# Kernel tuning notes

Hardware: AMD Instinct MI355X
Metric: run time of the kernel (lower is better)

## Reference

```python
import jax, jax.numpy as jnp
import numpy as np

K = 1024
D = 512
BETA = 0.25
ALPHA = 10.0
EPS_NORM = 1e-12  # torch F.normalize eps


def _l2_normalize(x):
    n = jnp.linalg.norm(x, axis=1, keepdims=True)
    return x / jnp.maximum(n, EPS_NORM)


def setup_inputs() -> dict:
    key = jax.random.key(0)
    k1, k2 = jax.random.split(key)
    latents = jax.random.normal(k1, (16384, D), dtype=jnp.float32)
    # nn.Embedding weight init: uniform(-1/K, 1/K)
    emb_weight = jax.random.uniform(k2, (K, D), dtype=jnp.float32,
                                    minval=-1.0 / K, maxval=1.0 / K)
    return {"latents": latents, "emb_weight": emb_weight}


def reference(latents, emb_weight):
    # latents: [B, D], emb_weight: [K, D]
    ln = _l2_normalize(latents)                               # [B, D]
    # torch uses embedding.weight.data -> detached for the attention path
    cb = _l2_normalize(jax.lax.stop_gradient(emb_weight))     # [K, D]
    attention = ln @ cb.T                                     # [B, K]
    soft_assign = jax.nn.softmax(ALPHA * attention, axis=1)   # [B, K]
    quantized = soft_assign @ emb_weight                      # [B, D]

    commitment_loss = jnp.mean((jax.lax.stop_gradient(quantized) - ln) ** 2)
    embedding_loss = jnp.mean((quantized - jax.lax.stop_gradient(ln)) ** 2)
    vq_loss = commitment_loss * BETA + embedding_loss

    avg_probs = jnp.mean(soft_assign, axis=0)                 # [K]
    entropy_vq = -jnp.sum(avg_probs * jnp.log(avg_probs + 1e-10))

    argm = jnp.argmax(attention, axis=1, keepdims=True)       # [B, 1] int
    one_hot = jax.nn.one_hot(argm[:, 0], K, dtype=latents.dtype)  # [B, K]
    hard_quantized = one_hot @ emb_weight                     # [B, D]
    # attention[one_hot.bool()].mean() == mean of row-max (argmax entries)
    cluster_metric = jnp.mean(jnp.max(attention, axis=1))

    return (quantized, vq_loss, entropy_vq, argm, hard_quantized,
            soft_assign, cluster_metric)
```

## Files before the change

### kernel.cpp

```cpp
#include <hip/hip_runtime.h>
#include <math.h>

#define D     512
#define KCB   1024
#define NT    256
#define NT2   512
#define ALPHA 10.0f
#define TAU   0.008f
#define PSTR  1040

typedef __attribute__((ext_vector_type(8))) short short8v;
typedef __attribute__((ext_vector_type(4))) float f32x4;
typedef unsigned short us;

__device__ __forceinline__ float wave_reduce_sum(float v) {
    #pragma unroll
    for (int off = 32; off >= 1; off >>= 1) v += __shfl_xor(v, off, 64);
    return v;
}

__device__ __forceinline__ short bf16r(float x) {
    union { float f; unsigned u; } c; c.f = x;
    unsigned r = (c.u + 0x7FFFu + ((c.u >> 16) & 1u)) >> 16;
    return (short)r;
}

__global__ void k_init(float* __restrict__ avg, float* __restrict__ sse, float* __restrict__ clu) {
    int t = threadIdx.x + blockIdx.x * blockDim.x;
    if (t < KCB) avg[t] = 0.0f;
    if (t == 0) { *sse = 0.0f; *clu = 0.0f; }
}

__global__ __launch_bounds__(NT) void k_prep(const float* __restrict__ emb,
                                             us* __restrict__ cb, float* __restrict__ cbinv) {
    const int k = blockIdx.x, t = threadIdx.x;
    const int wv = t >> 6, lane = t & 63;
    float2 v = ((const float2*)(emb + (size_t)k * D))[t];
    float ss = wave_reduce_sum(v.x * v.x + v.y * v.y);
    __shared__ float part[4];
    __shared__ float s_i;
    if (lane == 0) part[wv] = ss;
    __syncthreads();
    if (t == 0) s_i = 1.0f / fmaxf(sqrtf(part[0] + part[1] + part[2] + part[3]), 1e-12f);
    __syncthreads();
    float inv = s_i;
    unsigned lo = (unsigned short)bf16r(v.x * inv);
    unsigned hi = (unsigned short)bf16r(v.y * inv);
    const int d = 2 * t;
    size_t idx = (((size_t)(k >> 4) * 16 + (d >> 5)) * 64 + ((d >> 3) & 3) * 16 + (k & 15)) * 8 + (d & 7);
    ((unsigned*)cb)[idx >> 1] = lo | (hi << 16);
    if (t == 0) cbinv[k] = inv;
}

__global__ __launch_bounds__(NT) void k_tr(const float* __restrict__ emb, us* __restrict__ embT) {
    __shared__ us tile[64][65];
    const int t = threadIdx.x;
    const int k0 = (blockIdx.x & 15) * 64;
    const int d0 = (blockIdx.x >> 4) * 64;
    {
        const int r = t >> 2, cq = t & 3;
        const float4* ep = (const float4*)(emb + (size_t)(k0 + r) * D + d0 + cq * 16);
        float4 v0 = ep[0], v1 = ep[1], v2 = ep[2], v3 = ep[3];
        us* tp = &tile[r][cq * 16];
        tp[0] = (us)bf16r(v0.x); tp[1] = (us)bf16r(v0.y); tp[2] = (us)bf16r(v0.z); tp[3] = (us)bf16r(v0.w);
        tp[4] = (us)bf16r(v1.x); tp[5] = (us)bf16r(v1.y); tp[6] = (us)bf16r(v1.z); tp[7] = (us)bf16r(v1.w);
        tp[8] = (us)bf16r(v2.x); tp[9] = (us)bf16r(v2.y); tp[10] = (us)bf16r(v2.z); tp[11] = (us)bf16r(v2.w);
        tp[12] = (us)bf16r(v3.x); tp[13] = (us)bf16r(v3.y); tp[14] = (us)bf16r(v3.z); tp[15] = (us)bf16r(v3.w);
    }
    __syncthreads();
    {
        const int rd = t >> 2, kq = t & 3;
        const int dcol = d0 + rd;
        short8v w0, w1;
        #pragma unroll
        for (int j = 0; j < 8; ++j) w0[j] = (short)tile[kq * 16 + j][rd];
        #pragma unroll
        for (int j = 0; j < 8; ++j) w1[j] = (short)tile[kq * 16 + 8 + j][rd];
        const int kb0 = k0 + kq * 16, kb1 = kb0 + 8;
        size_t i0 = (((size_t)(dcol >> 4) * 32 + (kb0 >> 5)) * 64 + ((kb0 >> 3) & 3) * 16 + (dcol & 15)) * 8;
        size_t i1 = (((size_t)(dcol >> 4) * 32 + (kb1 >> 5)) * 64 + ((kb1 >> 3) & 3) * 16 + (dcol & 15)) * 8;
        *(short8v*)(embT + i0) = w0;
        *(short8v*)(embT + i1) = w1;
    }
}

__global__ __launch_bounds__(NT2, 2) void k_fused(
    const float* __restrict__ lat, const float* __restrict__ emb,
    const us* __restrict__ cb, const us* __restrict__ embT, const float* __restrict__ cbinv,
    float* __restrict__ avg_ws, float* __restrict__ clu_ws, float* __restrict__ sse_ws,
    float* __restrict__ q_out, float* __restrict__ soft_out,
    float* __restrict__ argm_out, float* __restrict__ hq_out)
{
    extern __shared__ __align__(16) us pool[];
    __shared__ float s_inv[32];
    __shared__ float s_maxp[8][32];
    __shared__ float s_amax[32];
    __shared__ float s_sump[8][32];
    __shared__ float s_den[32];
    __shared__ float s_bestv[32];
    __shared__ int   s_besti[32];
    __shared__ int   s_cnt;
    __shared__ int   s_ck[512];
    __shared__ float s_cv[512];
    __shared__ float part[8];

    const int t = threadIdx.x, wv = t >> 6, lane = t & 63;
    const int q15 = lane & 15, g = lane >> 4;
    const int b0 = blockIdx.x * 32;

    float4 ra[4], rb[4];
    #pragma unroll
    for (int i = 0; i < 4; ++i) {
        const float4* lp = (const float4*)(lat + (size_t)(b0 + wv * 4 + i) * D);
        ra[i] = lp[2 * lane]; rb[i] = lp[2 * lane + 1];
    }
    #pragma unroll
    for (int i = 0; i < 4; ++i) {
        int r = wv * 4 + i;
        float4 a = ra[i], b = rb[i];
        float ss = a.x*a.x + a.y*a.y + a.z*a.z + a.w*a.w
                 + b.x*b.x + b.y*b.y + b.z*b.z + b.w*b.w;
        ss = wave_reduce_sum(ss);
        float inv = 1.0f / fmaxf(sqrtf(ss), 1e-12f);
        short8v w;
        w[0] = bf16r(a.x * inv); w[1] = bf16r(a.y * inv);
        w[2] = bf16r(a.z * inv); w[3] = bf16r(a.w * inv);
        w[4] = bf16r(b.x * inv); w[5] = bf16r(b.y * inv);
        w[6] = bf16r(b.z * inv); w[7] = bf16r(b.w * inv);
        *(short8v*)&pool[(size_t)r * PSTR + lane * 8] = w;
        if (lane == 0) s_inv[r] = inv;
    }
    if (t == 0) s_cnt = 0;
    __syncthreads();

    f32x4 acc[2][8];
    #pragma unroll
    for (int m = 0; m < 2; ++m)
        #pragma unroll
        for (int ct = 0; ct < 8; ++ct) { f32x4 z = {0.f, 0.f, 0.f, 0.f}; acc[m][ct] = z; }

    const us* pBw = cb + (size_t)(wv * 8) * 16 * 512 + (size_t)lane * 8;
    #define LDB_A(ks, ct) (*(const short8v*)(pBw + (size_t)((ct) * 16 + (ks)) * 512))
    #define LDA_A(row, ks) (*(const short8v*)&pool[(size_t)(row) * PSTR + (ks) * 32 + g * 8])

    short8v bE[8], bO[8];
    #pragma unroll
    for (int ct = 0; ct < 8; ++ct) bE[ct] = LDB_A(0, ct);
    for (int ks = 0; ks < 16; ks += 2) {
        #pragma unroll
        for (int ct = 0; ct < 8; ++ct) bO[ct] = LDB_A(ks + 1, ct);
        short8v af0 = LDA_A(q15, ks), af1 = LDA_A(16 + q15, ks);
        #pragma unroll
        for (int ct = 0; ct < 8; ++ct) {
            acc[0][ct] = __builtin_amdgcn_mfma_f32_16x16x32_bf16(af0, bE[ct], acc[0][ct], 0, 0, 0);
            acc[1][ct] = __builtin_amdgcn_mfma_f32_16x16x32_bf16(af1, bE[ct], acc[1][ct], 0, 0, 0);
        }
        const int ksn = (ks + 2 < 16) ? ks + 2 : 0;
        #pragma unroll
        for (int ct = 0; ct < 8; ++ct) bE[ct] = LDB_A(ksn, ct);
        af0 = LDA_A(q15, ks + 1); af1 = LDA_A(16 + q15, ks + 1);
        #pragma unroll
        for (int ct = 0; ct < 8; ++ct) {
            acc[0][ct] = __builtin_amdgcn_mfma_f32_16x16x32_bf16(af0, bO[ct], acc[0][ct], 0, 0, 0);
            acc[1][ct] = __builtin_amdgcn_mfma_f32_16x16x32_bf16(af1, bO[ct], acc[1][ct], 0, 0, 0);
        }
    }

    #pragma unroll
    for (int m = 0; m < 2; ++m)
        #pragma unroll
        for (int i = 0; i < 4; ++i) {
            float v = acc[m][0][i];
            #pragma unroll
            for (int ct = 1; ct < 8; ++ct) v = fmaxf(v, acc[m][ct][i]);
            #pragma unroll
            for (int off = 8; off >= 1; off >>= 1) v = fmaxf(v, __shfl_xor(v, off, 64));
            if (q15 == 0) s_maxp[wv][m * 16 + g * 4 + i] = v;
        }
    __syncthreads();
    if (t < 32) {
        float v = s_maxp[0][t];
        #pragma unroll
        for (int w = 1; w < 8; ++w) v = fmaxf(v, s_maxp[w][t]);
        s_amax[t] = v;
    }
    __syncthreads();

    #pragma unroll
    for (int m = 0; m < 2; ++m)
        #pragma unroll
        for (int i = 0; i < 4; ++i) {
            const int row = m * 16 + g * 4 + i;
            const float thr = s_amax[row] - TAU;
            #pragma unroll
            for (int ct = 0; ct < 8; ++ct) {
                if (acc[m][ct][i] >= thr) {
                    int idx = atomicAdd(&s_cnt, 1);
                    if (idx < 512) s_ck[idx] = (row << 16) | (wv * 128 + ct * 16 + q15);
                }
            }
        }
    __syncthreads();
    const int cnt = (s_cnt < 512) ? s_cnt : 512;

    for (int e = wv; e < cnt; e += 8) {
        const int pk = s_ck[e];
        const int row = pk >> 16, kk = pk & 0xFFFF;
        const float4* lp = (const float4*)(lat + (size_t)(b0 + row) * D);
        const float4* ep = (const float4*)(emb + (size_t)kk * D);
        float4 x0 = lp[2 * lane], x1 = lp[2 * lane + 1];
        float4 y0 = ep[2 * lane], y1 = ep[2 * lane + 1];
        float dp = x0.x*y0.x + x0.y*y0.y + x0.z*y0.z + x0.w*y0.w
                 + x1.x*y1.x + x1.y*y1.y + x1.z*y1.z + x1.w*y1.w;
        dp = wave_reduce_sum(dp);
        if (lane == 0) s_cv[e] = dp * s_inv[row] * cbinv[kk];
    }
    __syncthreads();
    if (t < 32) {
        float bv = -1e30f; int bi = 0x7FFFFFFF;
        for (int e = 0; e < cnt; ++e) {
            if ((s_ck[e] >> 16) == t) {
                float v = s_cv[e]; int kk = s_ck[e] & 0xFFFF;
                if (v > bv || (v == bv && kk < bi)) { bv = v; bi = kk; }
            }
        }
        s_bestv[t] = bv; s_besti[t] = bi;
        argm_out[b0 + t] = (float)bi;
    }
    __syncthreads();

    #pragma unroll
    for (int m = 0; m < 2; ++m)
        #pragma unroll
        for (int i = 0; i < 4; ++i) {
            const float bvv = s_bestv[m * 16 + g * 4 + i];
            float s = 0.f;
            #pragma unroll
            for (int ct = 0; ct < 8; ++ct) {
                float e = __expf(ALPHA * (acc[m][ct][i] - bvv));
                acc[m][ct][i] = e;
                s += e;
            }
            #pragma unroll
            for (int off = 8; off >= 1; off >>= 1) s += __shfl_xor(s, off, 64);
            if (q15 == 0) s_sump[wv][m * 16 + g * 4 + i] = s;
        }
    __syncthreads();
    if (t < 32) {
        float s = s_sump[0][t];
        #pragma unroll
        for (int w = 1; w < 8; ++w) s += s_sump[w][t];
        s_den[t] = 1.0f / s;
    }
    __syncthreads();

    float csum[8];
    #pragma unroll
    for (int ct = 0; ct < 8; ++ct) csum[ct] = 0.f;
    #pragma unroll
    for (int m = 0; m < 2; ++m)
        #pragma unroll
        for (int i = 0; i < 4; ++i) {
            const int row = m * 16 + g * 4 + i;
            const float dn = s_den[row];
            float* orow = soft_out + (size_t)(b0 + row) * KCB + wv * 128 + q15;
            us* prow = &pool[(size_t)row * PSTR + wv * 128 + q15];
            #pragma unroll
            for (int ct = 0; ct < 8; ++ct) {
                float sv = acc[m][ct][i] * dn;
                orow[ct * 16] = sv;
                prow[ct * 16] = (us)bf16r(sv);
                csum[ct] += sv;
            }
        }
    #pragma unroll
    for (int ct = 0; ct < 8; ++ct) {
        float v = csum[ct];
        v += __shfl_xor(v, 16, 64);
        v += __shfl_xor(v, 32, 64);
        csum[ct] = v;
    }
    if (lane < 16) {
        #pragma unroll
        for (int ct = 0; ct < 8; ++ct)
            atomicAdd(avg_ws + wv * 128 + ct * 16 + lane, csum[ct]);
    }
    if (t == 0) {
        float cs = 0.f;
        #pragma unroll
        for (int r = 0; r < 32; ++r) cs += s_bestv[r];
        atomicAdd(clu_ws, cs);
    }
    __syncthreads();

    const float4* emb4 = (const float4*)emb;
    #pragma unroll
    for (int u = 0; u < 8; ++u) {
        int idx = t + u * NT2;
        int r = idx >> 7, c = idx & 127;
        ((float4*)(hq_out + (size_t)(b0 + r) * D))[c] = emb4[(size_t)s_besti[r] * 128 + c];
    }

    f32x4 qac[2][4];
    #pragma unroll
    for (int m = 0; m < 2; ++m)
        #pragma unroll
        for (int ct = 0; ct < 4; ++ct) { f32x4 z = {0.f, 0.f, 0.f, 0.f}; qac[m][ct] = z; }

    const us* pBq = embT + (size_t)(wv * 128) * 512 + (size_t)lane * 8;
    #define LDB_Q(ks, ct) (*(const short8v*)(pBq + (size_t)((ct) * 32 + (ks)) * 512))
    #define LDA_Q(row, ks) (*(const short8v*)&pool[(size_t)(row) * PSTR + (ks) * 32 + g * 8])

    short8v qE[4], qO[4];
    #pragma unroll
    for (int ct = 0; ct < 4; ++ct) qE[ct] = LDB_Q(0, ct);
    for (int ks = 0; ks < 32; ks += 2) {
        #pragma unroll
        for (int ct = 0; ct < 4; ++ct) qO[ct] = LDB_Q(ks + 1, ct);
        short8v af0 = LDA_Q(q15, ks), af1 = LDA_Q(16 + q15, ks);
        #pragma unroll
        for (int ct = 0; ct < 4; ++ct) {
            qac[0][ct] = __builtin_amdgcn_mfma_f32_16x16x32_bf16(af0, qE[ct], qac[0][ct], 0, 0, 0);
            qac[1][ct] = __builtin_amdgcn_mfma_f32_16x16x32_bf16(af1, qE[ct], qac[1][ct], 0, 0, 0);
        }
        const int ksn = (ks + 2 < 32) ? ks + 2 : 0;
        #pragma unroll
        for (int ct = 0; ct < 4; ++ct) qE[ct] = LDB_Q(ksn, ct);
        af0 = LDA_Q(q15, ks + 1); af1 = LDA_Q(16 + q15, ks + 1);
        #pragma unroll
        for (int ct = 0; ct < 4; ++ct) {
            qac[0][ct] = __builtin_amdgcn_mfma_f32_16x16x32_bf16(af0, qO[ct], qac[0][ct], 0, 0, 0);
            qac[1][ct] = __builtin_amdgcn_mfma_f32_16x16x32_bf16(af1, qO[ct], qac[1][ct], 0, 0, 0);
        }
    }

    float sse = 0.f;
    #pragma unroll
    for (int m = 0; m < 2; ++m)
        #pragma unroll
        for (int i = 0; i < 4; ++i) {
            const int rloc = m * 16 + g * 4 + i;
            const int row = b0 + rloc;
            const float rv = s_inv[rloc];
            const float* lrow = lat + (size_t)row * D + wv * 64 + q15;
            float* qrow = q_out + (size_t)row * D + wv * 64 + q15;
            #pragma unroll
            for (int ct = 0; ct < 4; ++ct) {
                float qv = qac[m][ct][i];
                qrow[ct * 16] = qv;
                float df = qv - lrow[ct * 16] * rv;
                sse += df * df;
            }
        }
    sse = wave_reduce_sum(sse);
    if (lane == 0) part[wv] = sse;
    __syncthreads();
    if (t == 0) {
        float s = 0.f;
        #pragma unroll
        for (int w = 0; w < 8; ++w) s += part[w];
        atomicAdd(sse_ws, s);
    }
    #undef LDB_A
    #undef LDA_A
    #undef LDB_Q
    #undef LDA_Q
}

__global__ __launch_bounds__(NT) void k_final(
    const float* __restrict__ avg_ws, const float* __restrict__ sse_ws, const float* __restrict__ clu_ws,
    float* __restrict__ out_vq, float* __restrict__ out_ent, float* __restrict__ out_cm,
    float invB, float invBD)
{
    const int t = threadIdx.x;
    float ent = 0.f;
    for (int idx = t; idx < KCB; idx += NT) {
        float pv = avg_ws[idx] * invB;
        ent -= pv * logf(pv + 1e-10f);
    }
    ent = wave_reduce_sum(ent);
    __shared__ float part[4];
    const int wv = t >> 6, lane = t & 63;
    if (lane == 0) part[wv] = ent;
    __syncthreads();
    if (t == 0) {
        *out_ent = part[0] + part[1] + part[2] + part[3];
        *out_vq  = 1.25f * (*sse_ws) * invBD;
        *out_cm  = (*clu_ws) * invB;
    }
}

extern "C" void kernel_launch(void* const* d_in, const int* in_sizes, int n_in,
                              void* d_out, int out_size, void* d_ws, size_t ws_size,
                              hipStream_t stream)
{
    const float* lat = (const float*)d_in[0];
    const float* emb = (const float*)d_in[1];
    const int B = in_sizes[0] / D;
    float* out = (float*)d_out;

    const size_t vq_off   = (size_t)B * D;
    const size_t ent_off  = vq_off + 1;
    const size_t argm_off = vq_off + 2;
    const size_t hq_off   = argm_off + (size_t)B;
    const size_t soft_off = hq_off + (size_t)B * D;
    const size_t cm_off   = soft_off + (size_t)B * KCB;

    us* cb_bf   = (us*)d_ws;
    us* embT_bf = cb_bf + (size_t)KCB * D;
    float* fbase  = (float*)(embT_bf + (size_t)D * KCB);
    float* cbinv  = fbase;
    float* avg_ws = cbinv + KCB;
    float* sse_ws = avg_ws + KCB;
    float* clu_ws = sse_ws + 1;

    const int lds_bytes = 32 * PSTR * 2;

    k_init<<<4, NT, 0, stream>>>(avg_ws, sse_ws, clu_ws);
    k_prep<<<KCB, NT, 0, stream>>>(emb, cb_bf, cbinv);
    k_tr<<<(D / 64) * (KCB / 64), NT, 0, stream>>>(emb, embT_bf);
    k_fused<<<B / 32, NT2, lds_bytes, stream>>>(lat, emb, cb_bf, embT_bf, cbinv,
                                                avg_ws, clu_ws, sse_ws,
                                                out, out + soft_off, out + argm_off, out + hq_off);
    k_final<<<1, NT, 0, stream>>>(avg_ws, sse_ws, clu_ws,
                                  out + vq_off, out + ent_off, out + cm_off,
                                  1.0f / (float)B, 1.0f / ((float)B * (float)D));
}
```

Before: 294.3 us.

## Double row tile to 64, merge prep kernels, and replace avg atomics with partials

The fused kernel now handles 64 latent rows per block instead of 32. Each codebook B-fragment loaded from global memory is reused across four M-tiles, which halves codebook traffic per row. The init, normalize and transpose prep kernels are merged into one launch that writes the transposed bf16 codebook with scattered 2-byte stores. Per-column soft-assignment sums go to a per-block partial buffer reduced by a new k_avg kernel when workspace allows, instead of global atomics. The cost is more accumulator registers, twice the LDS per block at a 2-block occupancy target, and half as many blocks.

```diff
diff --git a/kernel.cpp b/kernel.cpp
--- a/kernel.cpp
+++ b/kernel.cpp
@@ -5,6 +5,7 @@
 #define KCB   1024
 #define NT    256
 #define NT2   512
+#define RB    64
 #define ALPHA 10.0f
 #define TAU   0.008f
 #define PSTR  1040
@@ -25,16 +26,16 @@
     return (short)r;
 }
 
-__global__ void k_init(float* __restrict__ avg, float* __restrict__ sse, float* __restrict__ clu) {
-    int t = threadIdx.x + blockIdx.x * blockDim.x;
-    if (t < KCB) avg[t] = 0.0f;
-    if (t == 0) { *sse = 0.0f; *clu = 0.0f; }
-}
-
-__global__ __launch_bounds__(NT) void k_prep(const float* __restrict__ emb,
-                                             us* __restrict__ cb, float* __restrict__ cbinv) {
+__global__ __launch_bounds__(NT) void k_prep2(const float* __restrict__ emb,
+                                              us* __restrict__ cb, us* __restrict__ embT,
+                                              float* __restrict__ cbinv,
+                                              float* __restrict__ avg_ws,
+                                              float* __restrict__ sse, float* __restrict__ clu) {
     const int k = blockIdx.x, t = threadIdx.x;
     const int wv = t >> 6, lane = t & 63;
+    if (k < 4) avg_ws[k * NT + t] = 0.0f;
+    if (k == 0 && t == 0) { *sse = 0.0f; *clu = 0.0f; }
+
     float2 v = ((const float2*)(emb + (size_t)k * D))[t];
     float ss = wave_reduce_sum(v.x * v.x + v.y * v.y);
     __shared__ float part[4];
@@ -44,79 +45,51 @@
     if (t == 0) s_i = 1.0f / fmaxf(sqrtf(part[0] + part[1] + part[2] + part[3]), 1e-12f);
     __syncthreads();
     float inv = s_i;
+    const int d = 2 * t;
     unsigned lo = (unsigned short)bf16r(v.x * inv);
     unsigned hi = (unsigned short)bf16r(v.y * inv);
-    const int d = 2 * t;
     size_t idx = (((size_t)(k >> 4) * 16 + (d >> 5)) * 64 + ((d >> 3) & 3) * 16 + (k & 15)) * 8 + (d & 7);
     ((unsigned*)cb)[idx >> 1] = lo | (hi << 16);
+    size_t j0 = (((size_t)(d >> 4) * 32 + (k >> 5)) * 64 + ((k >> 3) & 3) * 16 + (d & 15)) * 8 + (k & 7);
+    embT[j0]     = (us)bf16r(v.x);
+    embT[j0 + 8] = (us)bf16r(v.y);
     if (t == 0) cbinv[k] = inv;
-}
-
-__global__ __launch_bounds__(NT) void k_tr(const float* __restrict__ emb, us* __restrict__ embT) {
-    __shared__ us tile[64][65];
-    const int t = threadIdx.x;
-    const int k0 = (blockIdx.x & 15) * 64;
-    const int d0 = (blockIdx.x >> 4) * 64;
-    {
-        const int r = t >> 2, cq = t & 3;
-        const float4* ep = (const float4*)(emb + (size_t)(k0 + r) * D + d0 + cq * 16);
-        float4 v0 = ep[0], v1 = ep[1], v2 = ep[2], v3 = ep[3];
-        us* tp = &tile[r][cq * 16];
-        tp[0] = (us)bf16r(v0.x); tp[1] = (us)bf16r(v0.y); tp[2] = (us)bf16r(v0.z); tp[3] = (us)bf16r(v0.w);
-        tp[4] = (us)bf16r(v1.x); tp[5] = (us)bf16r(v1.y); tp[6] = (us)bf16r(v1.z); tp[7] = (us)bf16r(v1.w);
-        tp[8] = (us)bf16r(v2.x); tp[9] = (us)bf16r(v2.y); tp[10] = (us)bf16r(v2.z); tp[11] = (us)bf16r(v2.w);
-        tp[12] = (us)bf16r(v3.x); tp[13] = (us)bf16r(v3.y); tp[14] = (us)bf16r(v3.z); tp[15] = (us)bf16r(v3.w);
-    }
-    __syncthreads();
-    {
-        const int rd = t >> 2, kq = t & 3;
-        const int dcol = d0 + rd;
-        short8v w0, w1;
-        #pragma unroll
-        for (int j = 0; j < 8; ++j) w0[j] = (short)tile[kq * 16 + j][rd];
-        #pragma unroll
-        for (int j = 0; j < 8; ++j) w1[j] = (short)tile[kq * 16 + 8 + j][rd];
-        const int kb0 = k0 + kq * 16, kb1 = kb0 + 8;
-        size_t i0 = (((size_t)(dcol >> 4) * 32 + (kb0 >> 5)) * 64 + ((kb0 >> 3) & 3) * 16 + (dcol & 15)) * 8;
-        size_t i1 = (((size_t)(dcol >> 4) * 32 + (kb1 >> 5)) * 64 + ((kb1 >> 3) & 3) * 16 + (dcol & 15)) * 8;
-        *(short8v*)(embT + i0) = w0;
-        *(short8v*)(embT + i1) = w1;
-    }
 }
 
 __global__ __launch_bounds__(NT2, 2) void k_fused(
     const float* __restrict__ lat, const float* __restrict__ emb,
     const us* __restrict__ cb, const us* __restrict__ embT, const float* __restrict__ cbinv,
-    float* __restrict__ avg_ws, float* __restrict__ clu_ws, float* __restrict__ sse_ws,
+    float* __restrict__ avg_ws, float* __restrict__ part_ws, int use_part,
+    float* __restrict__ clu_ws, float* __restrict__ sse_ws,
     float* __restrict__ q_out, float* __restrict__ soft_out,
     float* __restrict__ argm_out, float* __restrict__ hq_out)
 {
     extern __shared__ __align__(16) us pool[];
-    __shared__ float s_inv[32];
-    __shared__ float s_maxp[8][32];
-    __shared__ float s_amax[32];
-    __shared__ float s_sump[8][32];
-    __shared__ float s_den[32];
-    __shared__ float s_bestv[32];
-    __shared__ int   s_besti[32];
+    __shared__ float s_inv[RB];
+    __shared__ float s_maxp[8][RB];
+    __shared__ float s_amax[RB];
+    __shared__ float s_sump[8][RB];
+    __shared__ float s_den[RB];
+    __shared__ float s_bestv[RB];
+    __shared__ int   s_besti[RB];
     __shared__ int   s_cnt;
-    __shared__ int   s_ck[512];
-    __shared__ float s_cv[512];
+    __shared__ int   s_ck[1024];
+    __shared__ float s_cv[1024];
     __shared__ float part[8];
 
     const int t = threadIdx.x, wv = t >> 6, lane = t & 63;
     const int q15 = lane & 15, g = lane >> 4;
-    const int b0 = blockIdx.x * 32;
-
-    float4 ra[4], rb[4];
-    #pragma unroll
-    for (int i = 0; i < 4; ++i) {
-        const float4* lp = (const float4*)(lat + (size_t)(b0 + wv * 4 + i) * D);
+    const int b0 = blockIdx.x * RB;
+
+    float4 ra[8], rb[8];
+    #pragma unroll
+    for (int i = 0; i < 8; ++i) {
+        const float4* lp = (const float4*)(lat + (size_t)(b0 + wv * 8 + i) * D);
         ra[i] = lp[2 * lane]; rb[i] = lp[2 * lane + 1];
     }
     #pragma unroll
-    for (int i = 0; i < 4; ++i) {
-        int r = wv * 4 + i;
+    for (int i = 0; i < 8; ++i) {
+        int r = wv * 8 + i;
         float4 a = ra[i], b = rb[i];
         float ss = a.x*a.x + a.y*a.y + a.z*a.z + a.w*a.w
                  + b.x*b.x + b.y*b.y + b.z*b.z + b.w*b.w;
@@ -133,9 +106,9 @@
     if (t == 0) s_cnt = 0;
     __syncthreads();
 
-    f32x4 acc[2][8];
-    #pragma unroll
-    for (int m = 0; m < 2; ++m)
+    f32x4 acc[4][8];
+    #pragma unroll
+    for (int m = 0; m < 4; ++m)
         #pragma unroll
         for (int ct = 0; ct < 8; ++ct) { f32x4 z = {0.f, 0.f, 0.f, 0.f}; acc[m][ct] = z; }
 
@@ -149,25 +122,35 @@
     for (int ks = 0; ks < 16; ks += 2) {
         #pragma unroll
         for (int ct = 0; ct < 8; ++ct) bO[ct] = LDB_A(ks + 1, ct);
-        short8v af0 = LDA_A(q15, ks), af1 = LDA_A(16 + q15, ks);
-        #pragma unroll
-        for (int ct = 0; ct < 8; ++ct) {
-            acc[0][ct] = __builtin_amdgcn_mfma_f32_16x16x32_bf16(af0, bE[ct], acc[0][ct], 0, 0, 0);
-            acc[1][ct] = __builtin_amdgcn_mfma_f32_16x16x32_bf16(af1, bE[ct], acc[1][ct], 0, 0, 0);
+        {
+            short8v af0 = LDA_A(q15, ks), af1 = LDA_A(16 + q15, ks);
+            short8v af2 = LDA_A(32 + q15, ks), af3 = LDA_A(48 + q15, ks);
+            #pragma unroll
+            for (int ct = 0; ct < 8; ++ct) {
+                acc[0][ct] = __builtin_amdgcn_mfma_f32_16x16x32_bf16(af0, bE[ct], acc[0][ct], 0, 0, 0);
+                acc[1][ct] = __builtin_amdgcn_mfma_f32_16x16x32_bf16(af1, bE[ct], acc[1][ct], 0, 0, 0);
+                acc[2][ct] = __builtin_amdgcn_mfma_f32_16x16x32_bf16(af2, bE[ct], acc[2][ct], 0, 0, 0);
+                acc[3][ct] = __builtin_amdgcn_mfma_f32_16x16x32_bf16(af3, bE[ct], acc[3][ct], 0, 0, 0);
+            }
         }
         const int ksn = (ks + 2 < 16) ? ks + 2 : 0;
         #pragma unroll
         for (int ct = 0; ct < 8; ++ct) bE[ct] = LDB_A(ksn, ct);
-        af0 = LDA_A(q15, ks + 1); af1 = LDA_A(16 + q15, ks + 1);
-        #pragma unroll
-        for (int ct = 0; ct < 8; ++ct) {
-            acc[0][ct] = __builtin_amdgcn_mfma_f32_16x16x32_bf16(af0, bO[ct], acc[0][ct], 0, 0, 0);
-            acc[1][ct] = __builtin_amdgcn_mfma_f32_16x16x32_bf16(af1, bO[ct], acc[1][ct], 0, 0, 0);
-        }
-    }
-
-    #pragma unroll
-    for (int m = 0; m < 2; ++m)
+        {
+            short8v af0 = LDA_A(q15, ks + 1), af1 = LDA_A(16 + q15, ks + 1);
+            short8v af2 = LDA_A(32 + q15, ks + 1), af3 = LDA_A(48 + q15, ks + 1);
+            #pragma unroll
+            for (int ct = 0; ct < 8; ++ct) {
+                acc[0][ct] = __builtin_amdgcn_mfma_f32_16x16x32_bf16(af0, bO[ct], acc[0][ct], 0, 0, 0);
+                acc[1][ct] = __builtin_amdgcn_mfma_f32_16x16x32_bf16(af1, bO[ct], acc[1][ct], 0, 0, 0);
+                acc[2][ct] = __builtin_amdgcn_mfma_f32_16x16x32_bf16(af2, bO[ct], acc[2][ct], 0, 0, 0);
+                acc[3][ct] = __builtin_amdgcn_mfma_f32_16x16x32_bf16(af3, bO[ct], acc[3][ct], 0, 0, 0);
+            }
+        }
+    }
+
+    #pragma unroll
+    for (int m = 0; m < 4; ++m)
         #pragma unroll
         for (int i = 0; i < 4; ++i) {
             float v = acc[m][0][i];
@@ -178,7 +161,7 @@
             if (q15 == 0) s_maxp[wv][m * 16 + g * 4 + i] = v;
         }
     __syncthreads();
-    if (t < 32) {
+    if (t < RB) {
         float v = s_maxp[0][t];
         #pragma unroll
         for (int w = 1; w < 8; ++w) v = fmaxf(v, s_maxp[w][t]);
@@ -187,7 +170,7 @@
     __syncthreads();
 
     #pragma unroll
-    for (int m = 0; m < 2; ++m)
+    for (int m = 0; m < 4; ++m)
         #pragma unroll
         for (int i = 0; i < 4; ++i) {
             const int row = m * 16 + g * 4 + i;
@@ -196,12 +179,12 @@
             for (int ct = 0; ct < 8; ++ct) {
                 if (acc[m][ct][i] >= thr) {
                     int idx = atomicAdd(&s_cnt, 1);
-                    if (idx < 512) s_ck[idx] = (row << 16) | (wv * 128 + ct * 16 + q15);
+                    if (idx < 1024) s_ck[idx] = (row << 16) | (wv * 128 + ct * 16 + q15);
                 }
             }
         }
     __syncthreads();
-    const int cnt = (s_cnt < 512) ? s_cnt : 512;
+    const int cnt = (s_cnt < 1024) ? s_cnt : 1024;
 
     for (int e = wv; e < cnt; e += 8) {
         const int pk = s_ck[e];
@@ -216,7 +199,7 @@
         if (lane == 0) s_cv[e] = dp * s_inv[row] * cbinv[kk];
     }
     __syncthreads();
-    if (t < 32) {
+    if (t < RB) {
         float bv = -1e30f; int bi = 0x7FFFFFFF;
         for (int e = 0; e < cnt; ++e) {
             if ((s_ck[e] >> 16) == t) {
@@ -230,7 +213,7 @@
     __syncthreads();
 
     #pragma unroll
-    for (int m = 0; m < 2; ++m)
+    for (int m = 0; m < 4; ++m)
         #pragma unroll
         for (int i = 0; i < 4; ++i) {
             const float bvv = s_bestv[m * 16 + g * 4 + i];
@@ -246,7 +229,7 @@
             if (q15 == 0) s_sump[wv][m * 16 + g * 4 + i] = s;
         }
     __syncthreads();
-    if (t < 32) {
+    if (t < RB) {
         float s = s_sump[0][t];
         #pragma unroll
         for (int w = 1; w < 8; ++w) s += s_sump[w][t];
@@ -258,7 +241,7 @@
     #pragma unroll
     for (int ct = 0; ct < 8; ++ct) csum[ct] = 0.f;
     #pragma unroll
-    for (int m = 0; m < 2; ++m)
+    for (int m = 0; m < 4; ++m)
         #pragma unroll
         for (int i = 0; i < 4; ++i) {
             const int row = m * 16 + g * 4 + i;
@@ -280,30 +263,38 @@
         v += __shfl_xor(v, 32, 64);
         csum[ct] = v;
     }
-    if (lane < 16) {
-        #pragma unroll
-        for (int ct = 0; ct < 8; ++ct)
-            atomicAdd(avg_ws + wv * 128 + ct * 16 + lane, csum[ct]);
+    if (use_part) {
+        if (lane < 16) {
+            #pragma unroll
+            for (int ct = 0; ct < 8; ++ct)
+                part_ws[(size_t)blockIdx.x * KCB + wv * 128 + ct * 16 + lane] = csum[ct];
+        }
+    } else {
+        if (lane < 16) {
+            #pragma unroll
+            for (int ct = 0; ct < 8; ++ct)
+                atomicAdd(avg_ws + wv * 128 + ct * 16 + lane, csum[ct]);
+        }
     }
     if (t == 0) {
         float cs = 0.f;
         #pragma unroll
-        for (int r = 0; r < 32; ++r) cs += s_bestv[r];
+        for (int r = 0; r < RB; ++r) cs += s_bestv[r];
         atomicAdd(clu_ws, cs);
     }
     __syncthreads();
 
     const float4* emb4 = (const float4*)emb;
     #pragma unroll
-    for (int u = 0; u < 8; ++u) {
+    for (int u = 0; u < 16; ++u) {
         int idx = t + u * NT2;
         int r = idx >> 7, c = idx & 127;
         ((float4*)(hq_out + (size_t)(b0 + r) * D))[c] = emb4[(size_t)s_besti[r] * 128 + c];
     }
 
-    f32x4 qac[2][4];
-    #pragma unroll
-    for (int m = 0; m < 2; ++m)
+    f32x4 qac[4][4];
+    #pragma unroll
+    for (int m = 0; m < 4; ++m)
         #pragma unroll
         for (int ct = 0; ct < 4; ++ct) { f32x4 z = {0.f, 0.f, 0.f, 0.f}; qac[m][ct] = z; }
 
@@ -317,26 +308,36 @@
     for (int ks = 0; ks < 32; ks += 2) {
         #pragma unroll
         for (int ct = 0; ct < 4; ++ct) qO[ct] = LDB_Q(ks + 1, ct);
-        short8v af0 = LDA_Q(q15, ks), af1 = LDA_Q(16 + q15, ks);
-        #pragma unroll
-        for (int ct = 0; ct < 4; ++ct) {
-            qac[0][ct] = __builtin_amdgcn_mfma_f32_16x16x32_bf16(af0, qE[ct], qac[0][ct], 0, 0, 0);
-            qac[1][ct] = __builtin_amdgcn_mfma_f32_16x16x32_bf16(af1, qE[ct], qac[1][ct], 0, 0, 0);
+        {
+            short8v af0 = LDA_Q(q15, ks), af1 = LDA_Q(16 + q15, ks);
+            short8v af2 = LDA_Q(32 + q15, ks), af3 = LDA_Q(48 + q15, ks);
+            #pragma unroll
+            for (int ct = 0; ct < 4; ++ct) {
+                qac[0][ct] = __builtin_amdgcn_mfma_f32_16x16x32_bf16(af0, qE[ct], qac[0][ct], 0, 0, 0);
+                qac[1][ct] = __builtin_amdgcn_mfma_f32_16x16x32_bf16(af1, qE[ct], qac[1][ct], 0, 0, 0);
+                qac[2][ct] = __builtin_amdgcn_mfma_f32_16x16x32_bf16(af2, qE[ct], qac[2][ct], 0, 0, 0);
+                qac[3][ct] = __builtin_amdgcn_mfma_f32_16x16x32_bf16(af3, qE[ct], qac[3][ct], 0, 0, 0);
+            }
         }
         const int ksn = (ks + 2 < 32) ? ks + 2 : 0;
         #pragma unroll
         for (int ct = 0; ct < 4; ++ct) qE[ct] = LDB_Q(ksn, ct);
-        af0 = LDA_Q(q15, ks + 1); af1 = LDA_Q(16 + q15, ks + 1);
-        #pragma unroll
-        for (int ct = 0; ct < 4; ++ct) {
-            qac[0][ct] = __builtin_amdgcn_mfma_f32_16x16x32_bf16(af0, qO[ct], qac[0][ct], 0, 0, 0);
-            qac[1][ct] = __builtin_amdgcn_mfma_f32_16x16x32_bf16(af1, qO[ct], qac[1][ct], 0, 0, 0);
+        {
+            short8v af0 = LDA_Q(q15, ks + 1), af1 = LDA_Q(16 + q15, ks + 1);
+            short8v af2 = LDA_Q(32 + q15, ks + 1), af3 = LDA_Q(48 + q15, ks + 1);
+            #pragma unroll
+            for (int ct = 0; ct < 4; ++ct) {
+                qac[0][ct] = __builtin_amdgcn_mfma_f32_16x16x32_bf16(af0, qO[ct], qac[0][ct], 0, 0, 0);
+                qac[1][ct] = __builtin_amdgcn_mfma_f32_16x16x32_bf16(af1, qO[ct], qac[1][ct], 0, 0, 0);
+                qac[2][ct] = __builtin_amdgcn_mfma_f32_16x16x32_bf16(af2, qO[ct], qac[2][ct], 0, 0, 0);
+                qac[3][ct] = __builtin_amdgcn_mfma_f32_16x16x32_bf16(af3, qO[ct], qac[3][ct], 0, 0, 0);
+            }
         }
     }
 
     float sse = 0.f;
     #pragma unroll
-    for (int m = 0; m < 2; ++m)
+    for (int m = 0; m < 4; ++m)
         #pragma unroll
         for (int i = 0; i < 4; ++i) {
             const int rloc = m * 16 + g * 4 + i;
@@ -365,6 +366,16 @@
     #undef LDA_A
     #undef LDB_Q
     #undef LDA_Q
+}
+
+__global__ __launch_bounds__(NT) void k_avg(const float* __restrict__ part_ws, float* __restrict__ avg_ws,
+                                            int nblk) {
+    const int c  = (blockIdx.x & 3) * NT + threadIdx.x;
+    const int r0 = (blockIdx.x >> 2) * (nblk / 4);
+    const int r1 = r0 + nblk / 4;
+    float s = 0.f;
+    for (int r = r0; r < r1; ++r) s += part_ws[(size_t)r * KCB + c];
+    atomicAdd(avg_ws + c, s);
 }
 
 __global__ __launch_bounds__(NT) void k_final(
@@ -406,6 +417,8 @@
     const size_t soft_off = hq_off + (size_t)B * D;
     const size_t cm_off   = soft_off + (size_t)B * KCB;
 
+    const int nblk = B / RB;
+
     us* cb_bf   = (us*)d_ws;
     us* embT_bf = cb_bf + (size_t)KCB * D;
     float* fbase  = (float*)(embT_bf + (size_t)D * KCB);
@@ -413,15 +426,18 @@
     float* avg_ws = cbinv + KCB;
     float* sse_ws = avg_ws + KCB;
     float* clu_ws = sse_ws + 1;
-
-    const int lds_bytes = 32 * PSTR * 2;
-
-    k_init<<<4, NT, 0, stream>>>(avg_ws, sse_ws, clu_ws);
-    k_prep<<<KCB, NT, 0, stream>>>(emb, cb_bf, cbinv);
-    k_tr<<<(D / 64) * (KCB / 64), NT, 0, stream>>>(emb, embT_bf);
-    k_fused<<<B / 32, NT2, lds_bytes, stream>>>(lat, emb, cb_bf, embT_bf, cbinv,
-                                                avg_ws, clu_ws, sse_ws,
-                                                out, out + soft_off, out + argm_off, out + hq_off);
+    float* part_ws = clu_ws + 1;
+
+    const size_t base_bytes = (size_t)((char*)part_ws - (char*)d_ws);
+    const int use_part = (ws_size >= base_bytes + (size_t)nblk * KCB * 4) ? 1 : 0;
+
+    const int lds_bytes = RB * PSTR * 2;
+
+    k_prep2<<<KCB, NT, 0, stream>>>(emb, cb_bf, embT_bf, cbinv, avg_ws, sse_ws, clu_ws);
+    k_fused<<<nblk, NT2, lds_bytes, stream>>>(lat, emb, cb_bf, embT_bf, cbinv,
+                                              avg_ws, part_ws, use_part, clu_ws, sse_ws,
+                                              out, out + soft_off, out + argm_off, out + hq_off);
+    if (use_part) k_avg<<<16, NT, 0, stream>>>(part_ws, avg_ws, nblk);
     k_final<<<1, NT, 0, stream>>>(avg_ws, sse_ws, clu_ws,
                                   out + vq_off, out + ent_off, out + cm_off,
                                   1.0f / (float)B, 1.0f / ((float)B * (float)D));
```

After: 277.3 us. -5.8%, faster.
